# Kernel tuning notes

Hardware: AMD Instinct MI355X
Metric: run time of the kernel (lower is better)

## Reference

```python
import jax, jax.numpy as jnp
import numpy as np

BATCH, DIM, HEADS = 512, 2048, 16
CPH = DIM // HEADS  # per-head channels = 128
EPS = 1e-5


def setup_inputs() -> dict:
    key = jax.random.key(0)
    ks = jax.random.split(key, 6)
    x = jax.random.normal(ks[0], (BATCH, DIM, 1, 1), dtype=jnp.float32)
    W_qv = jax.random.normal(ks[1], (2 * DIM, DIM), dtype=jnp.float32) * (1.0 / np.sqrt(DIM))
    temperature = jnp.ones((HEADS, 1, 1), dtype=jnp.float32)
    k_param = jax.random.normal(ks[2], (BATCH, DIM, 1, 1), dtype=jnp.float32)
    bias_param = jax.random.normal(ks[3], (BATCH, HEADS, CPH * CPH, 1), dtype=jnp.float32)
    bn_gamma = jnp.ones((HEADS,), dtype=jnp.float32)
    bn_beta = jnp.zeros((HEADS,), dtype=jnp.float32)
    W_out = jax.random.normal(ks[4], (DIM, DIM, 1, 1), dtype=jnp.float32) * (1.0 / np.sqrt(DIM))
    b_out = jax.random.normal(ks[5], (DIM,), dtype=jnp.float32) * 0.01
    return {"x": x, "W_qv": W_qv, "temperature": temperature, "k_param": k_param,
            "bias_param": bias_param, "bn_gamma": bn_gamma, "bn_beta": bn_beta,
            "W_out": W_out, "b_out": b_out}


def reference(x, W_qv, temperature, k_param, bias_param, bn_gamma, bn_beta, W_out, b_out):
    b, c, h, w = x.shape  # h = w = 1 (required by x.squeeze() + Linear)
    heads = temperature.shape[0]
    cph = c // heads

    xs = x.reshape(b, c)
    qv = xs @ W_qv.T                     # [b, 2c]
    q, v = qv[:, :c], qv[:, c:]
    q = q.reshape(b, heads, cph, 1)      # b head c (h w)
    v = v.reshape(b, heads, cph, 1)
    k = k_param.reshape(b, heads, cph, 1)

    # BatchNorm2d over channel = head (training-mode batch stats, biased var)
    mean = jnp.mean(v, axis=(0, 2, 3), keepdims=True)
    var = jnp.var(v, axis=(0, 2, 3), keepdims=True)
    v = (v - mean) * jax.lax.rsqrt(var + EPS)
    v = v * bn_gamma.reshape(1, heads, 1, 1) + bn_beta.reshape(1, heads, 1, 1)

    # attn = q @ k^T over the singleton spatial dim -> [b, head, cph, cph]
    attn = jnp.einsum('bhcx,bhdx->bhcd', q, k)
    attn = attn + bias_param.reshape(b, heads, cph, cph)
    attn = attn * temperature  # [heads,1,1] broadcasts over batch
    attn = jax.nn.softmax(attn, axis=-1)

    out = jnp.einsum('bhcd,bhdx->bhcx', attn, v)  # [b, head, cph, 1]
    out = out.reshape(b, c)

    # 1x1 conv == matmul
    out = out @ W_out.reshape(c, c).T + b_out
    return out.reshape(b, c, 1, 1)
```

## Files before the change

### kernel.cpp

```cpp
#include <hip/hip_runtime.h>
#include <hip/hip_bf16.h>
#include <cstdint>

#define NBATCH 512
#define NDIM   2048
#define NHEADS 16
#define NCPH   128

typedef __bf16 bf16x8 __attribute__((ext_vector_type(8)));
typedef float  f32x4  __attribute__((ext_vector_type(4)));

__device__ __forceinline__ unsigned short f2bf(float f) {
    uint32_t u = __builtin_bit_cast(uint32_t, f);
    u += 0x7FFFu + ((u >> 16) & 1u);
    return (unsigned short)(u >> 16);
}

__device__ __forceinline__ void gl_lds16(const void* g, void* l) {
    __builtin_amdgcn_global_load_lds(
        (const __attribute__((address_space(1))) void*)g,
        (__attribute__((address_space(3))) void*)l,
        16, 0, 0);
}

__global__ __launch_bounds__(256) void cvt_all(
    const float* __restrict__ wqv, const float* __restrict__ wout,
    const float* __restrict__ x,
    unsigned short* __restrict__ owqv, unsigned short* __restrict__ owout,
    unsigned short* __restrict__ ox)
{
    int t = blockIdx.x * 256 + threadIdx.x;
    const int n1 = (2*NDIM*NDIM)/4;
    const int n2 = (NDIM*NDIM)/4;
    const float4* src; unsigned short* dst; int idx;
    if (t < n1)            { src = (const float4*)wqv;  dst = owqv;  idx = t; }
    else if (t < n1 + n2)  { src = (const float4*)wout; dst = owout; idx = t - n1; }
    else                   { src = (const float4*)x;    dst = ox;    idx = t - n1 - n2; }
    float4 v = src[idx];
    ushort4 o;
    o.x = f2bf(v.x); o.y = f2bf(v.y); o.z = f2bf(v.z); o.w = f2bf(v.w);
    *(ushort4*)(dst + (size_t)idx * 4) = o;
}

template<int BM, int BN, int BK, bool BNP>
__global__ __launch_bounds__(256) void gemm_bt(
    const unsigned short* __restrict__ A, const unsigned short* __restrict__ B,
    float* __restrict__ C, const float* __restrict__ bias,
    float* __restrict__ bnpart, int M, int N, int K)
{
    constexpr int WM = BM / 2, WN = BN / 2;
    constexpr int MI = WM / 16, NI = WN / 16;
    constexpr int NTA = (BM * BK) / 2048;
    constexpr int NTB = (BN * BK) / 2048;

    __shared__ unsigned short As[2][BM * BK];
    __shared__ unsigned short Bs[2][BN * BK];

    const int tid  = threadIdx.x;
    const int lane = tid & 63;
    const int wid  = tid >> 6;
    const int wr   = wid >> 1;
    const int wc   = wid & 1;
    const int m0   = blockIdx.y * BM;
    const int n0   = blockIdx.x * BN;
    const int fr   = lane & 15;
    const int kq   = lane >> 4;

    f32x4 acc[MI][NI] = {};

    auto stage = [&](int bs, int k0) {
#pragma unroll
        for (int r = 0; r < NTA; r++) {
            const int e   = r * 2048 + tid * 8;
            const int row = e / BK;
            const int swz = ((((e & (BK - 1)) >> 3) ^ (row & 7)) << 3);
            gl_lds16(A + (size_t)(m0 + row) * K + k0 + swz, &As[bs][e]);
        }
#pragma unroll
        for (int r = 0; r < NTB; r++) {
            const int e   = r * 2048 + tid * 8;
            const int row = e / BK;
            const int swz = ((((e & (BK - 1)) >> 3) ^ (row & 7)) << 3);
            gl_lds16(B + (size_t)(n0 + row) * K + k0 + swz, &Bs[bs][e]);
        }
    };

    auto compute = [&](int bs) {
#pragma unroll
        for (int kh = 0; kh < BK / 32; kh++) {
            const int kchunk = kh * 4 + kq;
            bf16x8 af[MI], bfv[NI];
#pragma unroll
            for (int i = 0; i < MI; i++) {
                const int row = wr * WM + i * 16 + fr;
                af[i] = *(const bf16x8*)&As[bs][row * BK + ((kchunk ^ (row & 7)) << 3)];
            }
#pragma unroll
            for (int j = 0; j < NI; j++) {
                const int row = wc * WN + j * 16 + fr;
                bfv[j] = *(const bf16x8*)&Bs[bs][row * BK + ((kchunk ^ (row & 7)) << 3)];
            }
#pragma unroll
            for (int i = 0; i < MI; i++)
#pragma unroll
                for (int j = 0; j < NI; j++)
                    acc[i][j] = __builtin_amdgcn_mfma_f32_16x16x32_bf16(
                        af[i], bfv[j], acc[i][j], 0, 0, 0);
        }
    };

    stage(0, 0);
    __syncthreads();

    const int NT = K / BK;
    int cur = 0;
    for (int t = 0; t < NT - 1; t++) {
        stage(cur ^ 1, (t + 1) * BK);
        compute(cur);
        __syncthreads();
        cur ^= 1;
    }
    compute(cur);

    const int row0 = m0 + wr * WM + (kq << 2);
    const int col0 = n0 + wc * WN + fr;
#pragma unroll
    for (int j = 0; j < NI; j++) {
        const int cc = col0 + j * 16;
        const float badd = bias ? bias[cc] : 0.0f;
#pragma unroll
        for (int i = 0; i < MI; i++)
#pragma unroll
            for (int r = 0; r < 4; r++)
                C[(size_t)(row0 + i * 16 + r) * N + cc] = acc[i][j][r] + badd;
    }

    if (BNP && n0 >= NDIM) {
        float s = 0.f, ss = 0.f;
#pragma unroll
        for (int i = 0; i < MI; i++)
#pragma unroll
            for (int j = 0; j < NI; j++)
#pragma unroll
                for (int r = 0; r < 4; r++) {
                    const float v = acc[i][j][r];
                    s += v;
                    ss = fmaf(v, v, ss);
                }
#pragma unroll
        for (int off = 32; off; off >>= 1) {
            s  += __shfl_down(s, off);
            ss += __shfl_down(ss, off);
        }
        __shared__ float rs[4], rss[4];
        if (lane == 0) { rs[wid] = s; rss[wid] = ss; }
        __syncthreads();
        if (tid == 0)
            ((float2*)bnpart)[((n0 - NDIM) >> 6) * 8 + (m0 >> 6)] =
                make_float2(rs[0] + rs[1] + rs[2] + rs[3],
                            rss[0] + rss[1] + rss[2] + rss[3]);
    }
}

__global__ __launch_bounds__(256) void bn_final(
    const float* __restrict__ bnpart, const float* __restrict__ gamma,
    const float* __restrict__ beta, float* __restrict__ sc2)
{
    const int t = threadIdx.x;
    float2 p = ((const float2*)bnpart)[t];
    float s = p.x, ss = p.y;
#pragma unroll
    for (int off = 8; off; off >>= 1) {
        s  += __shfl_down(s, off);
        ss += __shfl_down(ss, off);
    }
    if ((t & 15) == 0) {
        const int h = t >> 4;
        const float inv = 1.0f / (NBATCH * NCPH);
        float mean = s * inv;
        float var  = ss * inv - mean * mean;
        float sc   = gamma[h] * rsqrtf(var + 1e-5f);
        ((float2*)sc2)[h] = make_float2(sc, beta[h] - mean * sc);
    }
}

__global__ __launch_bounds__(256) void attn_k(
    const float* __restrict__ qv, const float* __restrict__ kparam,
    const float* __restrict__ bias, const float* __restrict__ temperature,
    const float* __restrict__ sc2, unsigned short* __restrict__ aout)
{
    const int bh = blockIdx.x;
    const int b  = bh >> 4;
    const int h  = bh & 15;
    const int tid = threadIdx.x;

    __shared__ float ks[NCPH], vsr[NCPH];
    if (tid < 32)
        ((float4*)ks)[tid] =
            ((const float4*)(kparam + (size_t)b * NDIM + h * NCPH))[tid];
    else if (tid < 64)
        ((float4*)vsr)[tid - 32] =
            ((const float4*)(qv + (size_t)b * (2 * NDIM) + NDIM + h * NCPH))[tid - 32];

    const int c = tid >> 1, half = tid & 1;
    const float qc   = qv[(size_t)b * (2 * NDIM) + h * NCPH + c];
    const float temp = temperature[h];
    const float2 s2  = ((const float2*)sc2)[h];

    const float4* bp = (const float4*)(bias + ((size_t)bh << 14)
                                       + (size_t)c * NCPH + half * 64);
    float4 l4[16];
#pragma unroll
    for (int j = 0; j < 16; j++) l4[j] = bp[j];

    __syncthreads();
    const float4* kk4 = (const float4*)(ks  + half * 64);
    const float4* vv4 = (const float4*)(vsr + half * 64);

    float s0 = 0.f, s1 = 0.f, o0 = 0.f, o1 = 0.f;
#pragma unroll
    for (int j = 0; j < 16; j++) {
        const float4 bb = l4[j];
        const float4 kx = kk4[j];
        const float4 vx = vv4[j];
        float px = __expf(fmaf(qc, kx.x, bb.x) * temp);
        float py = __expf(fmaf(qc, kx.y, bb.y) * temp);
        float pz = __expf(fmaf(qc, kx.z, bb.z) * temp);
        float pw = __expf(fmaf(qc, kx.w, bb.w) * temp);
        s0 += px; s1 += py; s0 += pz; s1 += pw;
        o0 = fmaf(px, vx.x, o0);
        o1 = fmaf(py, vx.y, o1);
        o0 = fmaf(pz, vx.z, o0);
        o1 = fmaf(pw, vx.w, o1);
    }
    float s = s0 + s1, o = o0 + o1;
    s += __shfl_xor(s, 1);
    o += __shfl_xor(o, 1);

    if (half == 0)
        aout[(size_t)b * NDIM + h * NCPH + c] = f2bf(fmaf(s2.x, o / s, s2.y));
}

extern "C" void kernel_launch(void* const* d_in, const int* in_sizes, int n_in,
                              void* d_out, int out_size, void* d_ws, size_t ws_size,
                              hipStream_t stream)
{
    const float* x      = (const float*)d_in[0];
    const float* Wqv    = (const float*)d_in[1];
    const float* temp   = (const float*)d_in[2];
    const float* kparam = (const float*)d_in[3];
    const float* bias   = (const float*)d_in[4];
    const float* gamma  = (const float*)d_in[5];
    const float* beta   = (const float*)d_in[6];
    const float* Wout   = (const float*)d_in[7];
    const float* bout   = (const float*)d_in[8];
    float* out = (float*)d_out;

    char* ws = (char*)d_ws;
    unsigned short* wqv_bf  = (unsigned short*)(ws);
    unsigned short* wout_bf = (unsigned short*)(ws + 16777216);
    unsigned short* x_bf    = (unsigned short*)(ws + 25165824);
    float*          qv      = (float*)(ws + 27262976);
    unsigned short* ao_bf   = (unsigned short*)(ws + 35651584);
    float*          bnpart  = (float*)(ws + 37748736);
    float*          sc2     = (float*)(ws + 37750784);

    cvt_all<<<13312, 256, 0, stream>>>(Wqv, Wout, x, wqv_bf, wout_bf, x_bf);

    gemm_bt<64, 64, 64, true><<<dim3(64, 8), 256, 0, stream>>>(
        x_bf, wqv_bf, qv, nullptr, bnpart, NBATCH, 2 * NDIM, NDIM);

    bn_final<<<1, 256, 0, stream>>>(bnpart, gamma, beta, sc2);

    attn_k<<<NBATCH * NHEADS, 256, 0, stream>>>(
        qv, kparam, bias, temp, sc2, ao_bf);

    gemm_bt<64, 32, 64, false><<<dim3(64, 8), 256, 0, stream>>>(
        ao_bf, wout_bf, out, bout, nullptr, NBATCH, NDIM, NDIM);
}
```

Measured before the change: 179.7 us.

## Fuse fp32-to-bf16 conversion into GEMM loads and fold BN finalize into attention

```diff
diff --git a/kernel.cpp b/kernel.cpp
--- a/kernel.cpp
+++ b/kernel.cpp
@@ -23,35 +23,19 @@
         16, 0, 0);
 }
 
-__global__ __launch_bounds__(256) void cvt_all(
-    const float* __restrict__ wqv, const float* __restrict__ wout,
-    const float* __restrict__ x,
-    unsigned short* __restrict__ owqv, unsigned short* __restrict__ owout,
-    unsigned short* __restrict__ ox)
-{
-    int t = blockIdx.x * 256 + threadIdx.x;
-    const int n1 = (2*NDIM*NDIM)/4;
-    const int n2 = (NDIM*NDIM)/4;
-    const float4* src; unsigned short* dst; int idx;
-    if (t < n1)            { src = (const float4*)wqv;  dst = owqv;  idx = t; }
-    else if (t < n1 + n2)  { src = (const float4*)wout; dst = owout; idx = t - n1; }
-    else                   { src = (const float4*)x;    dst = ox;    idx = t - n1 - n2; }
-    float4 v = src[idx];
-    ushort4 o;
-    o.x = f2bf(v.x); o.y = f2bf(v.y); o.z = f2bf(v.z); o.w = f2bf(v.w);
-    *(ushort4*)(dst + (size_t)idx * 4) = o;
-}
-
-template<int BM, int BN, int BK, bool BNP>
-__global__ __launch_bounds__(256) void gemm_bt(
-    const unsigned short* __restrict__ A, const unsigned short* __restrict__ B,
-    float* __restrict__ C, const float* __restrict__ bias,
-    float* __restrict__ bnpart, int M, int N, int K)
+template<int BM, int BN, int BK, bool A_BF16, bool BNP>
+__global__ __launch_bounds__(256) void gemm_f(
+    const unsigned short* __restrict__ Abf, const float* __restrict__ Af,
+    const float* __restrict__ Bf, float* __restrict__ C,
+    const float* __restrict__ bias, float* __restrict__ bnpart,
+    int M, int N, int K)
 {
     constexpr int WM = BM / 2, WN = BN / 2;
     constexpr int MI = WM / 16, NI = WN / 16;
-    constexpr int NTA = (BM * BK) / 2048;
-    constexpr int NTB = (BN * BK) / 2048;
+    constexpr int CPR = BK / 8;
+    constexpr int RA = (BM * BK) / 8 / 256;
+    constexpr int GA = (BM * BK) / 2048;
+    constexpr int RB = (BN * BK) / 8 / 256;
 
     __shared__ unsigned short As[2][BM * BK];
     __shared__ unsigned short Bs[2][BN * BK];
@@ -67,24 +51,68 @@
     const int kq   = lane >> 4;
 
     f32x4 acc[MI][NI] = {};
-
-    auto stage = [&](int bs, int k0) {
-#pragma unroll
-        for (int r = 0; r < NTA; r++) {
-            const int e   = r * 2048 + tid * 8;
-            const int row = e / BK;
-            const int swz = ((((e & (BK - 1)) >> 3) ^ (row & 7)) << 3);
-            gl_lds16(A + (size_t)(m0 + row) * K + k0 + swz, &As[bs][e]);
-        }
-#pragma unroll
-        for (int r = 0; r < NTB; r++) {
-            const int e   = r * 2048 + tid * 8;
-            const int row = e / BK;
-            const int swz = ((((e & (BK - 1)) >> 3) ^ (row & 7)) << 3);
-            gl_lds16(B + (size_t)(n0 + row) * K + k0 + swz, &Bs[bs][e]);
-        }
-    };
-
+    float4 rga[RA > 0 ? RA : 1][2], rgb[RB][2];
+
+    auto load_A = [&](int bs, int k0) {
+        if constexpr (A_BF16) {
+#pragma unroll
+            for (int r = 0; r < GA; r++) {
+                const int e   = r * 2048 + tid * 8;
+                const int row = e / BK;
+                const int swz = ((((e & (BK - 1)) >> 3) ^ (row & 7)) << 3);
+                gl_lds16(Abf + (size_t)(m0 + row) * K + k0 + swz, &As[bs][e]);
+            }
+        } else {
+#pragma unroll
+            for (int r = 0; r < RA; r++) {
+                const int idx = r * 256 + tid;
+                const int row = idx / CPR, cc = idx % CPR;
+                const float4* g = (const float4*)(Af + (size_t)(m0 + row) * K
+                                                  + k0 + cc * 8);
+                rga[r][0] = g[0];
+                rga[r][1] = g[1];
+            }
+        }
+    };
+    auto load_B = [&](int k0) {
+#pragma unroll
+        for (int r = 0; r < RB; r++) {
+            const int idx = r * 256 + tid;
+            const int row = idx / CPR, cc = idx % CPR;
+            const float4* g = (const float4*)(Bf + (size_t)(n0 + row) * K
+                                              + k0 + cc * 8);
+            rgb[r][0] = g[0];
+            rgb[r][1] = g[1];
+        }
+    };
+    auto write_A = [&](int bs) {
+        if constexpr (!A_BF16) {
+#pragma unroll
+            for (int r = 0; r < RA; r++) {
+                const int idx = r * 256 + tid;
+                const int row = idx / CPR, cc = idx % CPR;
+                bf16x8 v;
+                v[0] = (__bf16)rga[r][0].x; v[1] = (__bf16)rga[r][0].y;
+                v[2] = (__bf16)rga[r][0].z; v[3] = (__bf16)rga[r][0].w;
+                v[4] = (__bf16)rga[r][1].x; v[5] = (__bf16)rga[r][1].y;
+                v[6] = (__bf16)rga[r][1].z; v[7] = (__bf16)rga[r][1].w;
+                *(bf16x8*)&As[bs][row * BK + ((cc ^ (row & 7)) << 3)] = v;
+            }
+        }
+    };
+    auto write_B = [&](int bs) {
+#pragma unroll
+        for (int r = 0; r < RB; r++) {
+            const int idx = r * 256 + tid;
+            const int row = idx / CPR, cc = idx % CPR;
+            bf16x8 v;
+            v[0] = (__bf16)rgb[r][0].x; v[1] = (__bf16)rgb[r][0].y;
+            v[2] = (__bf16)rgb[r][0].z; v[3] = (__bf16)rgb[r][0].w;
+            v[4] = (__bf16)rgb[r][1].x; v[5] = (__bf16)rgb[r][1].y;
+            v[6] = (__bf16)rgb[r][1].z; v[7] = (__bf16)rgb[r][1].w;
+            *(bf16x8*)&Bs[bs][row * BK + ((cc ^ (row & 7)) << 3)] = v;
+        }
+    };
     auto compute = [&](int bs) {
 #pragma unroll
         for (int kh = 0; kh < BK / 32; kh++) {
@@ -93,12 +121,14 @@
 #pragma unroll
             for (int i = 0; i < MI; i++) {
                 const int row = wr * WM + i * 16 + fr;
-                af[i] = *(const bf16x8*)&As[bs][row * BK + ((kchunk ^ (row & 7)) << 3)];
+                af[i] = *(const bf16x8*)&As[bs][row * BK
+                        + ((kchunk ^ (row & 7)) << 3)];
             }
 #pragma unroll
             for (int j = 0; j < NI; j++) {
                 const int row = wc * WN + j * 16 + fr;
-                bfv[j] = *(const bf16x8*)&Bs[bs][row * BK + ((kchunk ^ (row & 7)) << 3)];
+                bfv[j] = *(const bf16x8*)&Bs[bs][row * BK
+                         + ((kchunk ^ (row & 7)) << 3)];
             }
 #pragma unroll
             for (int i = 0; i < MI; i++)
@@ -109,14 +139,20 @@
         }
     };
 
-    stage(0, 0);
+    load_A(0, 0);
+    load_B(0);
+    write_A(0);
+    write_B(0);
     __syncthreads();
 
     const int NT = K / BK;
     int cur = 0;
     for (int t = 0; t < NT - 1; t++) {
-        stage(cur ^ 1, (t + 1) * BK);
+        load_A(cur ^ 1, (t + 1) * BK);
+        load_B((t + 1) * BK);
         compute(cur);
+        write_A(cur ^ 1);
+        write_B(cur ^ 1);
         __syncthreads();
         cur ^= 1;
     }
@@ -162,39 +198,18 @@
     }
 }
 
-__global__ __launch_bounds__(256) void bn_final(
-    const float* __restrict__ bnpart, const float* __restrict__ gamma,
-    const float* __restrict__ beta, float* __restrict__ sc2)
-{
-    const int t = threadIdx.x;
-    float2 p = ((const float2*)bnpart)[t];
-    float s = p.x, ss = p.y;
-#pragma unroll
-    for (int off = 8; off; off >>= 1) {
-        s  += __shfl_down(s, off);
-        ss += __shfl_down(ss, off);
-    }
-    if ((t & 15) == 0) {
-        const int h = t >> 4;
-        const float inv = 1.0f / (NBATCH * NCPH);
-        float mean = s * inv;
-        float var  = ss * inv - mean * mean;
-        float sc   = gamma[h] * rsqrtf(var + 1e-5f);
-        ((float2*)sc2)[h] = make_float2(sc, beta[h] - mean * sc);
-    }
-}
-
 __global__ __launch_bounds__(256) void attn_k(
     const float* __restrict__ qv, const float* __restrict__ kparam,
     const float* __restrict__ bias, const float* __restrict__ temperature,
-    const float* __restrict__ sc2, unsigned short* __restrict__ aout)
+    const float* __restrict__ bnpart, const float* __restrict__ gamma,
+    const float* __restrict__ beta, unsigned short* __restrict__ aout)
 {
     const int bh = blockIdx.x;
     const int b  = bh >> 4;
     const int h  = bh & 15;
     const int tid = threadIdx.x;
 
-    __shared__ float ks[NCPH], vsr[NCPH];
+    __shared__ float ks[NCPH], vsr[NCPH], s2sh[2];
     if (tid < 32)
         ((float4*)ks)[tid] =
             ((const float4*)(kparam + (size_t)b * NDIM + h * NCPH))[tid];
@@ -202,10 +217,27 @@
         ((float4*)vsr)[tid - 32] =
             ((const float4*)(qv + (size_t)b * (2 * NDIM) + NDIM + h * NCPH))[tid - 32];
 
+    if (tid < 16) {
+        float2 p = ((const float2*)bnpart)[(h * 2 + (tid >> 3)) * 8 + (tid & 7)];
+        float s = p.x, ss = p.y;
+#pragma unroll
+        for (int off = 8; off; off >>= 1) {
+            s  += __shfl_xor(s, off);
+            ss += __shfl_xor(ss, off);
+        }
+        if (tid == 0) {
+            const float inv = 1.0f / (NBATCH * NCPH);
+            float mean = s * inv;
+            float var  = ss * inv - mean * mean;
+            float sc   = gamma[h] * rsqrtf(var + 1e-5f);
+            s2sh[0] = sc;
+            s2sh[1] = beta[h] - mean * sc;
+        }
+    }
+
     const int c = tid >> 1, half = tid & 1;
     const float qc   = qv[(size_t)b * (2 * NDIM) + h * NCPH + c];
     const float temp = temperature[h];
-    const float2 s2  = ((const float2*)sc2)[h];
 
     const float4* bp = (const float4*)(bias + ((size_t)bh << 14)
                                        + (size_t)c * NCPH + half * 64);
@@ -214,6 +246,7 @@
     for (int j = 0; j < 16; j++) l4[j] = bp[j];
 
     __syncthreads();
+    const float sc = s2sh[0], sh = s2sh[1];
     const float4* kk4 = (const float4*)(ks  + half * 64);
     const float4* vv4 = (const float4*)(vsr + half * 64);
 
@@ -238,7 +271,7 @@
     o += __shfl_xor(o, 1);
 
     if (half == 0)
-        aout[(size_t)b * NDIM + h * NCPH + c] = f2bf(fmaf(s2.x, o / s, s2.y));
+        aout[(size_t)b * NDIM + h * NCPH + c] = f2bf(fmaf(sc, o / s, sh));
 }
 
 extern "C" void kernel_launch(void* const* d_in, const int* in_sizes, int n_in,
@@ -257,24 +290,16 @@
     float* out = (float*)d_out;
 
     char* ws = (char*)d_ws;
-    unsigned short* wqv_bf  = (unsigned short*)(ws);
-    unsigned short* wout_bf = (unsigned short*)(ws + 16777216);
-    unsigned short* x_bf    = (unsigned short*)(ws + 25165824);
-    float*          qv      = (float*)(ws + 27262976);
-    unsigned short* ao_bf   = (unsigned short*)(ws + 35651584);
-    float*          bnpart  = (float*)(ws + 37748736);
-    float*          sc2     = (float*)(ws + 37750784);
-
-    cvt_all<<<13312, 256, 0, stream>>>(Wqv, Wout, x, wqv_bf, wout_bf, x_bf);
-
-    gemm_bt<64, 64, 64, true><<<dim3(64, 8), 256, 0, stream>>>(
-        x_bf, wqv_bf, qv, nullptr, bnpart, NBATCH, 2 * NDIM, NDIM);
-
-    bn_final<<<1, 256, 0, stream>>>(bnpart, gamma, beta, sc2);
+    float*          qv     = (float*)(ws);
+    unsigned short* ao_bf  = (unsigned short*)(ws + 8388608);
+    float*          bnpart = (float*)(ws + 10485760);
+
+    gemm_f<64, 64, 64, false, true><<<dim3(64, 8), 256, 0, stream>>>(
+        nullptr, x, Wqv, qv, nullptr, bnpart, NBATCH, 2 * NDIM, NDIM);
 
     attn_k<<<NBATCH * NHEADS, 256, 0, stream>>>(
-        qv, kparam, bias, temp, sc2, ao_bf);
-
-    gemm_bt<64, 32, 64, false><<<dim3(64, 8), 256, 0, stream>>>(
-        ao_bf, wout_bf, out, bout, nullptr, NBATCH, NDIM, NDIM);
-}
+        qv, kparam, bias, temp, bnpart, gamma, beta, ao_bf);
+
+    gemm_f<64, 32, 64, true, false><<<dim3(64, 8), 256, 0, stream>>>(
+        ao_bf, nullptr, Wout, out, bout, nullptr, NBATCH, NDIM, NDIM);
+}
```

After: 165.0 us. 1.09x faster.
